# Optimization experiments

Measured on AMD Instinct MI355X. Metric: run time of the kernel, lower is better.

Reference implementation:

```python
import jax, jax.numpy as jnp
import numpy as np

N_NODES = 100000
N_EDGES = 1600000
F_IN = 128
HID = 64
HORIZON = 100
NUM_TARGETS = 3


def setup_inputs() -> dict:
    key = jax.random.key(0)
    ks = jax.random.split(key, 7)
    x = jax.random.normal(ks[0], (N_NODES, F_IN), dtype=jnp.float32)
    edge_index = jax.random.randint(ks[1], (2, N_EDGES), 0, N_NODES, dtype=jnp.int64)
    s = 1.0 / np.sqrt(F_IN)
    W_l = jax.random.uniform(ks[2], (HID, F_IN), jnp.float32, -s, s)
    b_l = jax.random.uniform(ks[3], (HID,), jnp.float32, -s, s)
    W_r = jax.random.uniform(ks[4], (HID, F_IN), jnp.float32, -s, s)
    s2 = 1.0 / np.sqrt(HID)
    W_out = jax.random.uniform(ks[5], (NUM_TARGETS * HORIZON, HID), jnp.float32, -s2, s2)
    b_out = jax.random.uniform(ks[6], (NUM_TARGETS * HORIZON,), jnp.float32, -s2, s2)
    return {"x": x, "edge_index": edge_index, "W_l": W_l, "b_l": b_l,
            "W_r": W_r, "W_out": W_out, "b_out": b_out}


def reference(x, edge_index, W_l, b_l, W_r, W_out, b_out):
    n = x.shape[0]
    src, dst = edge_index[0], edge_index[1]
    # gather neighbor features and mean-aggregate per destination node
    msgs = x[src]  # [E, F_IN]
    agg = jax.ops.segment_sum(msgs, dst, num_segments=n)  # [N, F_IN]
    cnt = jax.ops.segment_sum(jnp.ones((edge_index.shape[1],), x.dtype), dst, num_segments=n)
    mean = agg / jnp.maximum(cnt, 1.0)[:, None]
    # SAGEConv: lin_l(aggregated) + lin_r(root), bias only on lin_l
    h = jnp.einsum('nf,hf->nh', mean, W_l) + b_l + jnp.einsum('nf,hf->nh', x, W_r)
    h = jax.nn.relu(h)
    out = jnp.einsum('nh,oh->no', h, W_out) + b_out  # [N, NUM_TARGETS*HORIZON]
    return out.reshape(-1, HORIZON)
```

## Files before the change

### kernel.cpp

```cpp
#include <hip/hip_runtime.h>

#define N_NODES 100000
#define F_IN 128
#define HID 64
#define OUT_F 300
#define WO_ROWS 320
#define NBKT 782
#define ECAP 2688
#define PART_BLOCKS 256
#define GEMM_BLOCKS 196
#define SORT_CAP 6400

typedef short bf8 __attribute__((ext_vector_type(8)));
typedef float f32x4 __attribute__((ext_vector_type(4)));

__device__ inline unsigned short f2bf(float f) {
    unsigned u = __builtin_bit_cast(unsigned, f);
    u += 0x7fff + ((u >> 16) & 1);
    return (unsigned short)(u >> 16);
}
__device__ inline float b2f(unsigned short h) {
    return __builtin_bit_cast(float, (unsigned)h << 16);
}

__global__ void k_prep(const float* __restrict__ Wl, const float* __restrict__ Wr,
                       const float* __restrict__ Wout,
                       unsigned short* __restrict__ Wc, unsigned short* __restrict__ Wo,
                       int* __restrict__ gcur) {
    int idx = blockIdx.x * blockDim.x + threadIdx.x;
    if (idx < 128 * 128) {
        int c = idx >> 7, k = idx & 127;
        float v = (c < HID) ? Wl[c * F_IN + k] : Wr[(c - HID) * F_IN + k];
        Wc[idx] = f2bf(v);
    } else if (idx < 128 * 128 + WO_ROWS * HID) {
        int j = idx - 128 * 128;
        int o = j >> 6, k = j & 63;
        Wo[j] = (o < OUT_F) ? f2bf(Wout[o * HID + k]) : (unsigned short)0;
    } else {
        int b = idx - 128 * 128 - WO_ROWS * HID;
        if (b < NBKT) gcur[b] = 0;
    }
}

__global__ __launch_bounds__(512) void k_pg(const int* __restrict__ ei,
                                            int* __restrict__ gcur,
                                            unsigned* __restrict__ pedges, int nE,
                                            const float* __restrict__ x,
                                            const unsigned short* __restrict__ Wc,
                                            unsigned short* __restrict__ yz) {
    if (blockIdx.x < PART_BLOCKS) {
        __shared__ unsigned sorted[SORT_CAP];
        __shared__ int hcnt[1024], hoff[1024], hcur[1024];
        __shared__ int wpre[8];
        const int tid = threadIdx.x, lane = tid & 63, wid = tid >> 6;
        const int per = (nE + PART_BLOCKS - 1) / PART_BLOCKS;
        const int e0 = blockIdx.x * per;
        const int e1 = min(e0 + per, nE);
        for (int cb = e0; cb < e1; cb += SORT_CAP) {
            const int cnt = min(SORT_CAP, e1 - cb);
            hcnt[tid * 2] = 0; hcnt[tid * 2 + 1] = 0;
            __syncthreads();
            for (int i = tid; i < cnt; i += 512)
                atomicAdd(&hcnt[ei[nE + cb + i] >> 7], 1);
            __syncthreads();
            int c0 = hcnt[tid * 2], c1 = hcnt[tid * 2 + 1];
            int tsum = c0 + c1;
            int s = tsum;
#pragma unroll
            for (int d = 1; d < 64; d <<= 1) { int t = __shfl_up(s, d, 64); if (lane >= d) s += t; }
            if (lane == 63) wpre[wid] = s;
            __syncthreads();
            if (tid == 0) { int run = 0; for (int w = 0; w < 8; ++w) { int t = wpre[w]; wpre[w] = run; run += t; } }
            __syncthreads();
            int excl = wpre[wid] + (s - tsum);
            hoff[tid * 2 + 0] = excl;       hcur[tid * 2 + 0] = excl;
            hoff[tid * 2 + 1] = excl + c0;  hcur[tid * 2 + 1] = excl + c0;
            __syncthreads();
            for (int i = tid; i < cnt; i += 512) {
                int src = ei[cb + i];
                int dst = ei[nE + cb + i];
                unsigned pk = ((unsigned)src << 7) | (unsigned)(dst & 127);
                int p = atomicAdd(&hcur[dst >> 7], 1);
                sorted[p] = pk;
            }
            __syncthreads();
            for (int b = tid; b < NBKT; b += 512) {
                int c = hcnt[b];
                if (c > 0) {
                    int gp = atomicAdd(&gcur[b], c);
                    unsigned* dst = pedges + (size_t)b * ECAP + gp;
                    int off = hoff[b];
                    for (int i = 0; i < c; ++i) dst[i] = sorted[off + i];
                }
            }
            __syncthreads();
        }
    } else {
        const int wv = threadIdx.x >> 6;
        const int nb = (blockIdx.x - PART_BLOCKS) * 512 + wv * 64;
        if (nb >= N_NODES) return;
        const int lane = threadIdx.x & 63;
        const int lm = lane & 15, lk = lane >> 4;

        f32x4 acc[4][8];
#pragma unroll
        for (int a = 0; a < 4; ++a)
#pragma unroll
            for (int b = 0; b < 8; ++b) acc[a][b] = f32x4{0.f, 0.f, 0.f, 0.f};

#pragma unroll
        for (int kt = 0; kt < 4; ++kt) {
            const int ko = kt * 32 + lk * 8;
            bf8 af[4], bw[8];
#pragma unroll
            for (int mt = 0; mt < 4; ++mt) {
                int row = nb + mt * 16 + lm;
                if (row >= N_NODES) row = N_NODES - 1;
                const float* xp = x + (size_t)row * F_IN + ko;
                float4 v0 = *(const float4*)xp;
                float4 v1 = *(const float4*)(xp + 4);
                bf8 t;
                t[0] = (short)f2bf(v0.x); t[1] = (short)f2bf(v0.y);
                t[2] = (short)f2bf(v0.z); t[3] = (short)f2bf(v0.w);
                t[4] = (short)f2bf(v1.x); t[5] = (short)f2bf(v1.y);
                t[6] = (short)f2bf(v1.z); t[7] = (short)f2bf(v1.w);
                af[mt] = t;
            }
#pragma unroll
            for (int nt = 0; nt < 8; ++nt)
                bw[nt] = *reinterpret_cast<const bf8*>(Wc + (nt * 16 + lm) * 128 + ko);
#pragma unroll
            for (int mt = 0; mt < 4; ++mt)
#pragma unroll
                for (int nt = 0; nt < 8; ++nt)
                    acc[mt][nt] = __builtin_amdgcn_mfma_f32_16x16x32_bf16(af[mt], bw[nt], acc[mt][nt], 0, 0, 0);
        }
#pragma unroll
        for (int mt = 0; mt < 4; ++mt)
#pragma unroll
            for (int r = 0; r < 4; ++r) {
                int node = nb + mt * 16 + lk * 4 + r;
                if (node < N_NODES) {
#pragma unroll
                    for (int nt = 0; nt < 8; ++nt)
                        yz[(size_t)node * 128 + nt * 16 + lm] = f2bf(acc[mt][nt][r]);
                }
            }
    }
}

__global__ __launch_bounds__(512) void k_agg3(const unsigned short* __restrict__ yz,
                                              const unsigned* __restrict__ pedges,
                                              const int* __restrict__ gcur,
                                              const float* __restrict__ bl,
                                              unsigned short* __restrict__ h) {
    __shared__ unsigned esrc[ECAP];
    __shared__ int hcnt[128], hoff[128], hcur[128];
    const int tid = threadIdx.x, lane = tid & 63, wv = tid >> 6;
    const int bkt = blockIdx.x;
    int cnt = gcur[bkt]; if (cnt > ECAP) cnt = ECAP;
    const size_t base = (size_t)bkt * ECAP;
    if (tid < 128) hcnt[tid] = 0;
    __syncthreads();
    for (int i = tid; i < cnt; i += 512)
        atomicAdd(&hcnt[pedges[base + i] & 127], 1);
    __syncthreads();
    if (tid < 64) {
        int a = hcnt[2 * tid], b = hcnt[2 * tid + 1];
        int s = a + b;
#pragma unroll
        for (int d = 1; d < 64; d <<= 1) { int t = __shfl_up(s, d, 64); if (lane >= d) s += t; }
        int ex = s - (a + b);
        hoff[2 * tid] = ex;     hcur[2 * tid] = ex;
        hoff[2 * tid + 1] = ex + a; hcur[2 * tid + 1] = ex + a;
    }
    __syncthreads();
    for (int i = tid; i < cnt; i += 512) {
        unsigned e = pedges[base + i];
        int p = atomicAdd(&hcur[e & 127], 1);
        esrc[p] = e >> 7;
    }
    __syncthreads();
    const int q = lane >> 4;
    const int f4 = (lane & 15) * 4;
    float4 blv = *(const float4*)(bl + f4);
    for (int loc = wv; loc < 128; loc += 8) {
        int node = bkt * 128 + loc;
        if (node >= N_NODES) break;
        int st = hoff[loc], dg = hcnt[loc];
        float s0 = 0.f, s1 = 0.f, s2 = 0.f, s3 = 0.f;
        int j = 0;
        for (; j + 8 <= dg; j += 8) {
            unsigned eA = esrc[st + j + q];
            unsigned eB = esrc[st + j + 4 + q];
            uint2 uA = *(const uint2*)(yz + (size_t)eA * 128 + f4);
            uint2 uB = *(const uint2*)(yz + (size_t)eB * 128 + f4);
            s0 += b2f(uA.x & 0xffff) + b2f(uB.x & 0xffff);
            s1 += b2f(uA.x >> 16)    + b2f(uB.x >> 16);
            s2 += b2f(uA.y & 0xffff) + b2f(uB.y & 0xffff);
            s3 += b2f(uA.y >> 16)    + b2f(uB.y >> 16);
        }
        if (j + 4 <= dg) {
            unsigned eA = esrc[st + j + q];
            uint2 uA = *(const uint2*)(yz + (size_t)eA * 128 + f4);
            s0 += b2f(uA.x & 0xffff);
            s1 += b2f(uA.x >> 16);
            s2 += b2f(uA.y & 0xffff);
            s3 += b2f(uA.y >> 16);
            j += 4;
        }
        int rem = dg - j;
        if (q < rem) {
            unsigned eA = esrc[st + j + q];
            uint2 uA = *(const uint2*)(yz + (size_t)eA * 128 + f4);
            s0 += b2f(uA.x & 0xffff);
            s1 += b2f(uA.x >> 16);
            s2 += b2f(uA.y & 0xffff);
            s3 += b2f(uA.y >> 16);
        }
        s0 += __shfl_xor(s0, 16); s0 += __shfl_xor(s0, 32);
        s1 += __shfl_xor(s1, 16); s1 += __shfl_xor(s1, 32);
        s2 += __shfl_xor(s2, 16); s2 += __shfl_xor(s2, 32);
        s3 += __shfl_xor(s3, 16); s3 += __shfl_xor(s3, 32);
        if (q == 0) {
            float inv = 1.0f / fmaxf((float)dg, 1.0f);
            uint2 zu = *(const uint2*)(yz + (size_t)node * 128 + HID + f4);
            float v0 = s0 * inv + b2f(zu.x & 0xffff) + blv.x;
            float v1 = s1 * inv + b2f(zu.x >> 16)    + blv.y;
            float v2 = s2 * inv + b2f(zu.y & 0xffff) + blv.z;
            float v3 = s3 * inv + b2f(zu.y >> 16)    + blv.w;
            uint2 hv;
            hv.x = (unsigned)f2bf(fmaxf(v0, 0.f)) | ((unsigned)f2bf(fmaxf(v1, 0.f)) << 16);
            hv.y = (unsigned)f2bf(fmaxf(v2, 0.f)) | ((unsigned)f2bf(fmaxf(v3, 0.f)) << 16);
            *(uint2*)(h + (size_t)node * HID + f4) = hv;
        }
    }
}

__global__ __launch_bounds__(256, 2) void k_fused2(
    const unsigned short* __restrict__ h, const unsigned short* __restrict__ Wo,
    const float* __restrict__ bout, float* __restrict__ out) {

    __shared__ float sout[64 * OUT_F];
    const int tid = threadIdx.x;
    const int lane = tid & 63;
    const int mt = tid >> 6;
    const int nb = blockIdx.x * 64;
    const int lm = lane & 15, lk = lane >> 4;

    int row = nb + mt * 16 + lm;
    if (row >= N_NODES) row = N_NODES - 1;
    bf8 ah[2];
#pragma unroll
    for (int k2 = 0; k2 < 2; ++k2)
        ah[k2] = *reinterpret_cast<const bf8*>(h + (size_t)row * HID + k2 * 32 + lk * 8);

    for (int g = 0; g < 5; ++g) {
        f32x4 acc2[4];
#pragma unroll
        for (int b = 0; b < 4; ++b) acc2[b] = f32x4{0.f, 0.f, 0.f, 0.f};
#pragma unroll
        for (int k2 = 0; k2 < 2; ++k2) {
            bf8 bw[4];
#pragma unroll
            for (int nt = 0; nt < 4; ++nt)
                bw[nt] = *reinterpret_cast<const bf8*>(
                    Wo + (size_t)((g * 4 + nt) * 16 + lm) * HID + k2 * 32 + lk * 8);
#pragma unroll
            for (int nt = 0; nt < 4; ++nt)
                acc2[nt] = __builtin_amdgcn_mfma_f32_16x16x32_bf16(ah[k2], bw[nt], acc2[nt], 0, 0, 0);
        }
#pragma unroll
        for (int nt = 0; nt < 4; ++nt) {
            int o = g * 64 + nt * 16 + lm;
            if (o < OUT_F) {
                float bo = bout[o];
#pragma unroll
                for (int r = 0; r < 4; ++r) {
                    int locn = mt * 16 + lk * 4 + r;
                    sout[locn * OUT_F + o] = acc2[nt][r] + bo;
                }
            }
        }
    }
    __syncthreads();
    const int nvalid = min(64, N_NODES - nb);
    const int total = nvalid * OUT_F;
    float* op = out + (size_t)nb * OUT_F;
    for (int i = tid; i < total; i += 256) op[i] = sout[i];
}

extern "C" void kernel_launch(void* const* d_in, const int* in_sizes, int n_in,
                              void* d_out, int out_size, void* d_ws, size_t ws_size,
                              hipStream_t stream) {
    const float* x    = (const float*)d_in[0];
    const int*   ei   = (const int*)d_in[1];
    const float* Wl   = (const float*)d_in[2];
    const float* bl   = (const float*)d_in[3];
    const float* Wr   = (const float*)d_in[4];
    const float* Wout = (const float*)d_in[5];
    const float* bout = (const float*)d_in[6];
    float* out = (float*)d_out;

    int nE = in_sizes[1] / 2;

    unsigned short* yz = (unsigned short*)d_ws;
    unsigned short* h  = yz + (size_t)N_NODES * 128;
    unsigned* pedges = (unsigned*)(h + (size_t)N_NODES * HID);
    int* gcur  = (int*)(pedges + (size_t)NBKT * ECAP);
    unsigned short* Wc = (unsigned short*)(gcur + NBKT);
    unsigned short* Wo = Wc + 128 * 128;

    int prep_n = 128 * 128 + WO_ROWS * HID + NBKT;
    k_prep<<<(prep_n + 255) / 256, 256, 0, stream>>>(Wl, Wr, Wout, Wc, Wo, gcur);
    k_pg<<<PART_BLOCKS + GEMM_BLOCKS, 512, 0, stream>>>(ei, gcur, pedges, nE, x, Wc, yz);
    k_agg3<<<NBKT, 512, 0, stream>>>(yz, pedges, gcur, bl, h);
    k_fused2<<<(N_NODES + 63) / 64, 256, 0, stream>>>(h, Wo, bout, out);
}
```

Baseline: 134.7 us.

## Fuse aggregation with output projection via LDS-resident hidden tile

Merges the aggregation kernel and the output GEMM into one kernel: each 128-node bucket writes its ReLU hidden vectors to shared memory, then the 8 waves compute the 300-wide output projection directly with swapped MFMA operands so each lane stores float4 rows straight to global. This removes the h round trip through global memory, one kernel launch, and the LDS staging buffer of the old output kernel. Separately, the x@W GEMM blocks are halved in rows per wave and doubled in count to spread that work over more CUs. Risks include higher LDS use per block, which lowers occupancy in the aggregation kernel, and output stores that are less coalesced than the old staged copy.

```diff
diff --git a/kernel.cpp b/kernel.cpp
--- a/kernel.cpp
+++ b/kernel.cpp
@@ -8,8 +8,9 @@
 #define NBKT 782
 #define ECAP 2688
 #define PART_BLOCKS 256
-#define GEMM_BLOCKS 196
+#define GEMM_BLOCKS 391
 #define SORT_CAP 6400
+#define HS 72
 
 typedef short bf8 __attribute__((ext_vector_type(8)));
 typedef float f32x4 __attribute__((ext_vector_type(4)));
@@ -97,23 +98,23 @@
         }
     } else {
         const int wv = threadIdx.x >> 6;
-        const int nb = (blockIdx.x - PART_BLOCKS) * 512 + wv * 64;
+        const int nb = (blockIdx.x - PART_BLOCKS) * 256 + wv * 32;
         if (nb >= N_NODES) return;
         const int lane = threadIdx.x & 63;
         const int lm = lane & 15, lk = lane >> 4;
 
-        f32x4 acc[4][8];
-#pragma unroll
-        for (int a = 0; a < 4; ++a)
+        f32x4 acc[2][8];
+#pragma unroll
+        for (int a = 0; a < 2; ++a)
 #pragma unroll
             for (int b = 0; b < 8; ++b) acc[a][b] = f32x4{0.f, 0.f, 0.f, 0.f};
 
 #pragma unroll
         for (int kt = 0; kt < 4; ++kt) {
             const int ko = kt * 32 + lk * 8;
-            bf8 af[4], bw[8];
-#pragma unroll
-            for (int mt = 0; mt < 4; ++mt) {
+            bf8 af[2], bw[8];
+#pragma unroll
+            for (int mt = 0; mt < 2; ++mt) {
                 int row = nb + mt * 16 + lm;
                 if (row >= N_NODES) row = N_NODES - 1;
                 const float* xp = x + (size_t)row * F_IN + ko;
@@ -130,13 +131,13 @@
             for (int nt = 0; nt < 8; ++nt)
                 bw[nt] = *reinterpret_cast<const bf8*>(Wc + (nt * 16 + lm) * 128 + ko);
 #pragma unroll
-            for (int mt = 0; mt < 4; ++mt)
+            for (int mt = 0; mt < 2; ++mt)
 #pragma unroll
                 for (int nt = 0; nt < 8; ++nt)
                     acc[mt][nt] = __builtin_amdgcn_mfma_f32_16x16x32_bf16(af[mt], bw[nt], acc[mt][nt], 0, 0, 0);
         }
 #pragma unroll
-        for (int mt = 0; mt < 4; ++mt)
+        for (int mt = 0; mt < 2; ++mt)
 #pragma unroll
             for (int r = 0; r < 4; ++r) {
                 int node = nb + mt * 16 + lk * 4 + r;
@@ -149,13 +150,16 @@
     }
 }
 
-__global__ __launch_bounds__(512) void k_agg3(const unsigned short* __restrict__ yz,
-                                              const unsigned* __restrict__ pedges,
-                                              const int* __restrict__ gcur,
-                                              const float* __restrict__ bl,
-                                              unsigned short* __restrict__ h) {
+__global__ __launch_bounds__(512) void k_aggout(const unsigned short* __restrict__ yz,
+                                                const unsigned* __restrict__ pedges,
+                                                const int* __restrict__ gcur,
+                                                const float* __restrict__ bl,
+                                                const unsigned short* __restrict__ Wo,
+                                                const float* __restrict__ bout,
+                                                float* __restrict__ out) {
     __shared__ unsigned esrc[ECAP];
     __shared__ int hcnt[128], hoff[128], hcur[128];
+    __shared__ __align__(16) unsigned short h_lds[128 * HS];
     const int tid = threadIdx.x, lane = tid & 63, wv = tid >> 6;
     const int bkt = blockIdx.x;
     int cnt = gcur[bkt]; if (cnt > ECAP) cnt = ECAP;
@@ -232,28 +236,17 @@
             uint2 hv;
             hv.x = (unsigned)f2bf(fmaxf(v0, 0.f)) | ((unsigned)f2bf(fmaxf(v1, 0.f)) << 16);
             hv.y = (unsigned)f2bf(fmaxf(v2, 0.f)) | ((unsigned)f2bf(fmaxf(v3, 0.f)) << 16);
-            *(uint2*)(h + (size_t)node * HID + f4) = hv;
-        }
-    }
-}
-
-__global__ __launch_bounds__(256, 2) void k_fused2(
-    const unsigned short* __restrict__ h, const unsigned short* __restrict__ Wo,
-    const float* __restrict__ bout, float* __restrict__ out) {
-
-    __shared__ float sout[64 * OUT_F];
-    const int tid = threadIdx.x;
-    const int lane = tid & 63;
-    const int mt = tid >> 6;
-    const int nb = blockIdx.x * 64;
+            *(uint2*)(h_lds + loc * HS + f4) = hv;
+        }
+    }
+    __syncthreads();
     const int lm = lane & 15, lk = lane >> 4;
-
-    int row = nb + mt * 16 + lm;
-    if (row >= N_NODES) row = N_NODES - 1;
+    const int nodeL = wv * 16 + lm;
+    const int node_g = bkt * 128 + nodeL;
     bf8 ah[2];
 #pragma unroll
     for (int k2 = 0; k2 < 2; ++k2)
-        ah[k2] = *reinterpret_cast<const bf8*>(h + (size_t)row * HID + k2 * 32 + lk * 8);
+        ah[k2] = *reinterpret_cast<const bf8*>(h_lds + nodeL * HS + k2 * 32 + lk * 8);
 
     for (int g = 0; g < 5; ++g) {
         f32x4 acc2[4];
@@ -268,26 +261,22 @@
                     Wo + (size_t)((g * 4 + nt) * 16 + lm) * HID + k2 * 32 + lk * 8);
 #pragma unroll
             for (int nt = 0; nt < 4; ++nt)
-                acc2[nt] = __builtin_amdgcn_mfma_f32_16x16x32_bf16(ah[k2], bw[nt], acc2[nt], 0, 0, 0);
+                acc2[nt] = __builtin_amdgcn_mfma_f32_16x16x32_bf16(bw[nt], ah[k2], acc2[nt], 0, 0, 0);
         }
 #pragma unroll
         for (int nt = 0; nt < 4; ++nt) {
-            int o = g * 64 + nt * 16 + lm;
-            if (o < OUT_F) {
-                float bo = bout[o];
-#pragma unroll
-                for (int r = 0; r < 4; ++r) {
-                    int locn = mt * 16 + lk * 4 + r;
-                    sout[locn * OUT_F + o] = acc2[nt][r] + bo;
-                }
-            }
-        }
-    }
-    __syncthreads();
-    const int nvalid = min(64, N_NODES - nb);
-    const int total = nvalid * OUT_F;
-    float* op = out + (size_t)nb * OUT_F;
-    for (int i = tid; i < total; i += 256) op[i] = sout[i];
+            int ob = (g * 4 + nt) * 16 + lk * 4;
+            if (ob + 3 < OUT_F && node_g < N_NODES) {
+                float4 bo = *(const float4*)(bout + ob);
+                float4 v;
+                v.x = acc2[nt][0] + bo.x;
+                v.y = acc2[nt][1] + bo.y;
+                v.z = acc2[nt][2] + bo.z;
+                v.w = acc2[nt][3] + bo.w;
+                *(float4*)(out + (size_t)node_g * OUT_F + ob) = v;
+            }
+        }
+    }
 }
 
 extern "C" void kernel_launch(void* const* d_in, const int* in_sizes, int n_in,
@@ -305,8 +294,7 @@
     int nE = in_sizes[1] / 2;
 
     unsigned short* yz = (unsigned short*)d_ws;
-    unsigned short* h  = yz + (size_t)N_NODES * 128;
-    unsigned* pedges = (unsigned*)(h + (size_t)N_NODES * HID);
+    unsigned* pedges = (unsigned*)(yz + (size_t)N_NODES * 128);
     int* gcur  = (int*)(pedges + (size_t)NBKT * ECAP);
     unsigned short* Wc = (unsigned short*)(gcur + NBKT);
     unsigned short* Wo = Wc + 128 * 128;
@@ -314,6 +302,5 @@
     int prep_n = 128 * 128 + WO_ROWS * HID + NBKT;
     k_prep<<<(prep_n + 255) / 256, 256, 0, stream>>>(Wl, Wr, Wout, Wc, Wo, gcur);
     k_pg<<<PART_BLOCKS + GEMM_BLOCKS, 512, 0, stream>>>(ei, gcur, pedges, nE, x, Wc, yz);
-    k_agg3<<<NBKT, 512, 0, stream>>>(yz, pedges, gcur, bl, h);
-    k_fused2<<<(N_NODES + 63) / 64, 256, 0, stream>>>(h, Wo, bout, out);
-}
+    k_aggout<<<NBKT, 512, 0, stream>>>(yz, pedges, gcur, bl, Wo, bout, out);
+}
```

Result: slower. 142.5 us (+5.8%).
